# Kernel optimization log

Hardware: AMD Instinct MI355X
Metric: run time of the kernel (lower is better)

## Reference

```python
import jax, jax.numpy as jnp
import numpy as np

BLOCK = 32           # sparsity_config.block
STRIDE_BLOCKS = 4    # stride 128 // block 32
B, H, L, HD = 2, 16, 4096, 64


def _make_fixed_layout(nb, bs):
    """DeepSpeed 'fixed' unidirectional layout, numverts=vertsize=1 (same for all heads)."""
    lay = np.zeros((nb, nb), dtype=np.int64)
    # local: lower-triangular within each stride window
    for i in range(0, nb, bs):
        for j in range(i, i + bs):
            lay[j, i:j + 1] = 1
    # global: vertical stripe at column offset bs-1 of every window, causal (col < row)
    start = bs - 1
    for i in range(nb):
        for j in range(start, i, bs):
            lay[i, j] = 1
    rows, cols = np.nonzero(lay)  # sorted by row
    return jnp.asarray(rows, jnp.int32), jnp.asarray(cols, jnp.int32)


def setup_inputs() -> dict:
    key = jax.random.key(0)
    kq, kk, kv = jax.random.split(key, 3)
    query = jax.random.normal(kq, (B, H, L, HD), jnp.float32)
    key_t = jax.random.normal(kk, (B, H, L, HD), jnp.float32)
    value = jax.random.normal(kv, (B, H, L, HD), jnp.float32)
    rows, cols = _make_fixed_layout(L // BLOCK, STRIDE_BLOCKS)
    return {"query": query, "key": key_t, "value": value,
            "rows": rows, "cols": cols, "block": BLOCK}


def reference(query, key, value, rows, cols, block):
    b, h, l, hd = query.shape
    nb = l // block
    scale = float(hd) ** (-0.5)
    # [nb, B, H, block, hd] with block-row axis leading for gather/scatter
    qb = jnp.moveaxis(query.reshape(b, h, nb, block, hd), 2, 0)
    kb = jnp.moveaxis(key.reshape(b, h, nb, block, hd), 2, 0)
    vb = jnp.moveaxis(value.reshape(b, h, nb, block, hd), 2, 0)
    # sdd: scores only on active blocks -> [nnz, B, H, block, block]
    s = jnp.einsum('nbhqd,nbhkd->nbhqk', qb[rows], kb[cols]) * scale
    # block-sparse softmax over each query row (segment reduce over blocks sharing a row)
    m_blk = s.max(-1)  # [nnz, B, H, block]
    row_max = jnp.full((nb, b, h, block), -jnp.inf, s.dtype).at[rows].max(m_blk)
    e = jnp.exp(s - row_max[rows][..., None])
    denom = jnp.zeros((nb, b, h, block), s.dtype).at[rows].add(e.sum(-1))
    p = e / denom[rows][..., None]
    # dsd: probs @ value, scatter-add into block rows
    ob = jnp.zeros((nb, b, h, block, hd), s.dtype).at[rows].add(
        jnp.einsum('nbhqk,nbhkd->nbhqd', p, vb[cols]))
    return jnp.moveaxis(ob, 0, 2).reshape(b, h, l, hd)
```

## Files before the change

### kernel.cpp

```cpp
#include <hip/hip_runtime.h>
#include <math.h>

#define BH    32
#define LSEQ  4096
#define HD    64
#define BLK   32
#define NB    128
#define NWIN  32
#define QSCALE 0.18033688011112042f

#define KSTR 34
#define VSTR 17

#define RAW_BARRIER() asm volatile("s_waitcnt lgkmcnt(0)\n\ts_barrier" ::: "memory")

typedef _Float16 h2  __attribute__((ext_vector_type(2)));
typedef _Float16 h8  __attribute__((ext_vector_type(8)));
typedef float    f16v __attribute__((ext_vector_type(16)));

static __device__ __forceinline__ h2 pk(float a, float b) {
    return __builtin_bit_cast(h2, __builtin_amdgcn_cvt_pkrtz(a, b));
}
static __device__ __forceinline__ unsigned pku(float a, float b) {
    return __builtin_bit_cast(unsigned, __builtin_amdgcn_cvt_pkrtz(a, b));
}
static __device__ __forceinline__ short h16(float x) {
    return __builtin_bit_cast(short, (_Float16)x);
}
static __device__ __forceinline__ h8 mk8(h2 a, h2 b, h2 c, h2 d) {
    h8 r;
    r[0] = a[0]; r[1] = a[1]; r[2] = b[0]; r[3] = b[1];
    r[4] = c[0]; r[5] = c[1]; r[6] = d[0]; r[7] = d[1];
    return r;
}

__global__ __launch_bounds__(128)
void sparse_attn_r2f(const float* __restrict__ Q, const float* __restrict__ K,
                     const float* __restrict__ V, float* __restrict__ out)
{
    const int id = (int)blockIdx.x;
    const int cc = id & 255;
    const int kk = id >> 8;
    const int v  = cc & 31;
    const int u  = cc >> 5;
    const int bh = u + 8 * kk;
    int w;
    switch (kk) {
        case 0:  w = v;              break;
        case 1:  w = (47 - v) & 31;  break;
        case 2:  w = (v + 16) & 31;  break;
        default: w = (63 - v) & 31;  break;
    }

    const int t    = (int)threadIdx.x;
    const int wid  = t >> 6;
    const int lane = t & 63;
    const int l31  = lane & 31;
    const int h    = lane >> 5;
    const int d0   = 2 * wid, d1 = 2 * wid + 1;
    const int r0   = 4 * w + d0, r1 = r0 + 1;

    __shared__ __align__(16) unsigned kbuf[2][BLK * KSTR];
    __shared__ __align__(16) unsigned vbuf[2][HD * VSTR];

    const size_t base = (size_t)bh * (LSEQ * HD);

    h8 qf0[4], qf1[4];
    {
        const float* qp0 = Q + base + (size_t)(r0 * BLK + l31) * HD + 8 * h;
        const float* qp1 = Q + base + (size_t)(r1 * BLK + l31) * HD + 8 * h;
#pragma unroll
        for (int tt = 0; tt < 4; ++tt) {
            float4 a = *(const float4*)(qp0 + 16 * tt);
            float4 b = *(const float4*)(qp0 + 16 * tt + 4);
            qf0[tt] = mk8(pk(a.x * QSCALE, a.y * QSCALE), pk(a.z * QSCALE, a.w * QSCALE),
                          pk(b.x * QSCALE, b.y * QSCALE), pk(b.z * QSCALE, b.w * QSCALE));
            float4 c = *(const float4*)(qp1 + 16 * tt);
            float4 e = *(const float4*)(qp1 + 16 * tt + 4);
            qf1[tt] = mk8(pk(c.x * QSCALE, c.y * QSCALE), pk(c.z * QSCALE, c.w * QSCALE),
                          pk(e.x * QSCALE, e.y * QSCALE), pk(e.z * QSCALE, e.w * QSCALE));
        }
    }

    f16v o00 = {}, o01 = {}, o10 = {}, o11 = {};
    float2 ls0 = make_float2(0.0f, 0.0f);
    float2 ls1 = make_float2(0.0f, 0.0f);

    const int n    = w + 4;
    const int srow = t >> 2;
    const int sdg  = t & 3;

    const float* kgb = K + base + (size_t)srow * HD + sdg * 16;
    const float* vgb = V + base + (size_t)srow * HD + sdg * 16;

    float4 kq0, kq1, kq2, kq3, vq0, vq1, vq2, vq3;

    auto loadR = [&](int j) {
        const int col = (j < w) ? (4 * j + 3) : (4 * w + (j - w));
        const size_t off = (size_t)col * (BLK * HD);
        kq0 = *(const float4*)(kgb + off);
        kq1 = *(const float4*)(kgb + off + 4);
        kq2 = *(const float4*)(kgb + off + 8);
        kq3 = *(const float4*)(kgb + off + 12);
        vq0 = *(const float4*)(vgb + off);
        vq1 = *(const float4*)(vgb + off + 4);
        vq2 = *(const float4*)(vgb + off + 8);
        vq3 = *(const float4*)(vgb + off + 12);
    };
    auto writeL = [&](int b) {
        unsigned* kb = &kbuf[b][srow * KSTR + sdg * 8];
        uint2 w0, w1, w2, w3;
        w0.x = pku(kq0.x, kq0.y); w0.y = pku(kq0.z, kq0.w);
        w1.x = pku(kq1.x, kq1.y); w1.y = pku(kq1.z, kq1.w);
        w2.x = pku(kq2.x, kq2.y); w2.y = pku(kq2.z, kq2.w);
        w3.x = pku(kq3.x, kq3.y); w3.y = pku(kq3.z, kq3.w);
        *(uint2*)&kb[0] = w0;
        *(uint2*)&kb[2] = w1;
        *(uint2*)&kb[4] = w2;
        *(uint2*)&kb[6] = w3;
        short* vs = (short*)&vbuf[b][0];
        const int vd0 = sdg * 16;
        vs[(vd0 +  0) * (2 * VSTR) + srow] = h16(vq0.x);
        vs[(vd0 +  1) * (2 * VSTR) + srow] = h16(vq0.y);
        vs[(vd0 +  2) * (2 * VSTR) + srow] = h16(vq0.z);
        vs[(vd0 +  3) * (2 * VSTR) + srow] = h16(vq0.w);
        vs[(vd0 +  4) * (2 * VSTR) + srow] = h16(vq1.x);
        vs[(vd0 +  5) * (2 * VSTR) + srow] = h16(vq1.y);
        vs[(vd0 +  6) * (2 * VSTR) + srow] = h16(vq1.z);
        vs[(vd0 +  7) * (2 * VSTR) + srow] = h16(vq1.w);
        vs[(vd0 +  8) * (2 * VSTR) + srow] = h16(vq2.x);
        vs[(vd0 +  9) * (2 * VSTR) + srow] = h16(vq2.y);
        vs[(vd0 + 10) * (2 * VSTR) + srow] = h16(vq2.z);
        vs[(vd0 + 11) * (2 * VSTR) + srow] = h16(vq2.w);
        vs[(vd0 + 12) * (2 * VSTR) + srow] = h16(vq3.x);
        vs[(vd0 + 13) * (2 * VSTR) + srow] = h16(vq3.y);
        vs[(vd0 + 14) * (2 * VSTR) + srow] = h16(vq3.z);
        vs[(vd0 + 15) * (2 * VSTR) + srow] = h16(vq3.w);
    };

    auto smpv = [&](const f16v& st, float2& ls, f16v& oa, f16v& ob,
                    const h8& vf00, const h8& vf01,
                    const h8& vf10, const h8& vf11) {
        float ps[16];
#pragma unroll
        for (int g = 0; g < 16; ++g) ps[g] = __builtin_exp2f(st[g]);
#pragma unroll
        for (int g = 0; g < 8; ++g) {
            ls.x += ps[2 * g];
            ls.y += ps[2 * g + 1];
        }
        h2 ph2[8];
#pragma unroll
        for (int jj = 0; jj < 8; ++jj) ph2[jj] = pk(ps[2 * jj], ps[2 * jj + 1]);
#pragma unroll
        for (int t2 = 0; t2 < 2; ++t2) {
            h2 s0 = h ? ph2[4 * t2]     : ph2[4 * t2 + 2];
            h2 s1 = h ? ph2[4 * t2 + 1] : ph2[4 * t2 + 3];
            int i0 = __shfl_xor(__builtin_bit_cast(int, s0), 32);
            int i1 = __shfl_xor(__builtin_bit_cast(int, s1), 32);
            h2 g0 = __builtin_bit_cast(h2, i0), g1 = __builtin_bit_cast(h2, i1);
            h2 c0 = h ? g0 : ph2[4 * t2];
            h2 c1 = h ? g1 : ph2[4 * t2 + 1];
            h2 c2 = h ? ph2[4 * t2 + 2] : g0;
            h2 c3 = h ? ph2[4 * t2 + 3] : g1;
            h8 pa = mk8(c0, c1, c2, c3);
            oa = __builtin_amdgcn_mfma_f32_32x32x16_f16(pa, t2 ? vf10 : vf00, oa, 0, 0, 0);
            ob = __builtin_amdgcn_mfma_f32_32x32x16_f16(pa, t2 ? vf11 : vf01, ob, 0, 0, 0);
        }
    };

    loadR(0);
    int pb = 0;

    for (int j = 0; j < n; ++j, pb ^= 1) {
        writeL(pb);
        if (j + 1 < n) loadR(j + 1);
        RAW_BARRIER();

        const int jj = j - w;
        const bool act1 = (jj < 0) || (jj <= d1);
        const bool act0 = (jj < 0) || (jj <= d0);
        if (act1) {
            const unsigned* kb = kbuf[pb];
            const unsigned* vb = vbuf[pb];

            f16v st0 = {}, st1 = {};
#pragma unroll
            for (int tt = 0; tt < 4; ++tt) {
                const int kw = l31 * KSTR + 8 * tt + 4 * h;
                uint2 u0 = *(const uint2*)&kb[kw];
                uint2 u1 = *(const uint2*)&kb[kw + 2];
                uint4 uu; uu.x = u0.x; uu.y = u0.y; uu.z = u1.x; uu.w = u1.y;
                h8 kf = __builtin_bit_cast(h8, uu);
                st1 = __builtin_amdgcn_mfma_f32_32x32x16_f16(kf, qf1[tt], st1, 0, 0, 0);
                st0 = __builtin_amdgcn_mfma_f32_32x32x16_f16(kf, qf0[tt], st0, 0, 0, 0);
            }

            const int va = l31 * VSTR + 4 * h;
            const int vc = (32 + l31) * VSTR + 4 * h;
            uint4 x00, x01, x10, x11;
            x00.x = vb[va];     x00.y = vb[va + 1];  x00.z = vb[va + 2];  x00.w = vb[va + 3];
            x01.x = vb[vc];     x01.y = vb[vc + 1];  x01.z = vb[vc + 2];  x01.w = vb[vc + 3];
            x10.x = vb[va + 8]; x10.y = vb[va + 9];  x10.z = vb[va + 10]; x10.w = vb[va + 11];
            x11.x = vb[vc + 8]; x11.y = vb[vc + 9];  x11.z = vb[vc + 10]; x11.w = vb[vc + 11];
            h8 vf00 = __builtin_bit_cast(h8, x00);
            h8 vf01 = __builtin_bit_cast(h8, x01);
            h8 vf10 = __builtin_bit_cast(h8, x10);
            h8 vf11 = __builtin_bit_cast(h8, x11);

            smpv(st1, ls1, o10, o11, vf00, vf01, vf10, vf11);
            if (act0) smpv(st0, ls0, o00, o01, vf00, vf01, vf10, vf11);
        }
    }

    auto finish = [&](float2 ls, const f16v& oa, const f16v& ob, int r) {
        float lsum = ls.x + ls.y;
        lsum += __shfl_xor(lsum, 32);
        const float inv = 1.0f / lsum;
        float* op = out + base + (size_t)(r * BLK) * HD;
#pragma unroll
        for (int g = 0; g < 16; ++g) {
            const int qrow = (g & 3) + 8 * (g >> 2) + 4 * h;
            int iv = __builtin_amdgcn_ds_bpermute(qrow << 2, __float_as_int(inv));
            const float invq = __int_as_float(iv);
            op[(size_t)qrow * HD + l31]      = oa[g] * invq;
            op[(size_t)qrow * HD + 32 + l31] = ob[g] * invq;
        }
    };
    finish(ls0, o00, o01, r0);
    finish(ls1, o10, o11, r1);
}

extern "C" void kernel_launch(void* const* d_in, const int* in_sizes, int n_in,
                              void* d_out, int out_size, void* d_ws, size_t ws_size,
                              hipStream_t stream) {
    const float* Q = (const float*)d_in[0];
    const float* K = (const float*)d_in[1];
    const float* V = (const float*)d_in[2];

    dim3 grid(NWIN * BH);
    dim3 block(128);
    sparse_attn_r2f<<<grid, block, 0, stream>>>(Q, K, V, (float*)d_out);
}
```

Before: 173.7 us.

## Split window work into single-wave blocks with barrier-free LDS double buffering

Each 128-thread block handling four block-rows of a window is replaced by two 64-thread single-wave blocks, each handling two block-rows and iterating only over the column blocks it needs. With one wave per block, the LDS barrier is removed. Global loads are prefetched two steps ahead and LDS writes one step ahead. The V tile row order is permuted so the P-matrix fragment can feed the PV MFMA directly without the cross-lane shuffle. This trades duplicated K/V loading across the two halves for more blocks, less wasted work on the diagonal, and no block-level synchronisation.

After: 172.4 us. Within noise of the previous version (-0.8%).

```diff
diff --git a/kernel.cpp b/kernel.cpp
--- a/kernel.cpp
+++ b/kernel.cpp
@@ -12,8 +12,6 @@
 #define KSTR 34
 #define VSTR 17
 
-#define RAW_BARRIER() asm volatile("s_waitcnt lgkmcnt(0)\n\ts_barrier" ::: "memory")
-
 typedef _Float16 h2  __attribute__((ext_vector_type(2)));
 typedef _Float16 h8  __attribute__((ext_vector_type(8)));
 typedef float    f16v __attribute__((ext_vector_type(16)));
@@ -34,31 +32,35 @@
     return r;
 }
 
-__global__ __launch_bounds__(128)
-void sparse_attn_r2f(const float* __restrict__ Q, const float* __restrict__ K,
-                     const float* __restrict__ V, float* __restrict__ out)
+__global__ __launch_bounds__(64, 2)
+void sparse_attn_pw(const float* __restrict__ Q, const float* __restrict__ K,
+                    const float* __restrict__ V, float* __restrict__ out)
 {
     const int id = (int)blockIdx.x;
     const int cc = id & 255;
-    const int kk = id >> 8;
+    const int s  = id >> 8;
     const int v  = cc & 31;
     const int u  = cc >> 5;
-    const int bh = u + 8 * kk;
+    const int q  = s >> 1;
+    const int half = s & 1;
     int w;
-    switch (kk) {
+    switch (q) {
         case 0:  w = v;              break;
         case 1:  w = (47 - v) & 31;  break;
         case 2:  w = (v + 16) & 31;  break;
         default: w = (63 - v) & 31;  break;
     }
-
-    const int t    = (int)threadIdx.x;
-    const int wid  = t >> 6;
-    const int lane = t & 63;
-    const int l31  = lane & 31;
-    const int h    = lane >> 5;
-    const int d0   = 2 * wid, d1 = 2 * wid + 1;
-    const int r0   = 4 * w + d0, r1 = r0 + 1;
+    const int bh = u + 8 * q;
+
+    const int t   = (int)threadIdx.x;
+    const int l31 = t & 31;
+    const int h   = t >> 5;
+    const int t15 = t & 15;
+    const int tr4 = t >> 4;
+
+    const int d0 = 2 * half, d1 = d0 + 1;
+    const int r0 = 4 * w + d0, r1 = r0 + 1;
+    const int n  = w + 2 + 2 * half;
 
     __shared__ __align__(16) unsigned kbuf[2][BLK * KSTR];
     __shared__ __align__(16) unsigned vbuf[2][HD * VSTR];
@@ -86,61 +88,44 @@
     float2 ls0 = make_float2(0.0f, 0.0f);
     float2 ls1 = make_float2(0.0f, 0.0f);
 
-    const int n    = w + 4;
-    const int srow = t >> 2;
-    const int sdg  = t & 3;
-
-    const float* kgb = K + base + (size_t)srow * HD + sdg * 16;
-    const float* vgb = V + base + (size_t)srow * HD + sdg * 16;
-
-    float4 kq0, kq1, kq2, kq3, vq0, vq1, vq2, vq3;
-
-    auto loadR = [&](int j) {
-        const int col = (j < w) ? (4 * j + 3) : (4 * w + (j - w));
-        const size_t off = (size_t)col * (BLK * HD);
-        kq0 = *(const float4*)(kgb + off);
-        kq1 = *(const float4*)(kgb + off + 4);
-        kq2 = *(const float4*)(kgb + off + 8);
-        kq3 = *(const float4*)(kgb + off + 12);
-        vq0 = *(const float4*)(vgb + off);
-        vq1 = *(const float4*)(vgb + off + 4);
-        vq2 = *(const float4*)(vgb + off + 8);
-        vq3 = *(const float4*)(vgb + off + 12);
+    float4 kst[8], vst[8];
+    const float* kg = K + base + (size_t)(tr4 * HD) + 4 * t15;
+    const float* vg = V + base + (size_t)(tr4 * HD) + 4 * t15;
+
+    auto colOf = [&](int j) { return (j < w) ? (4 * j + 3) : (4 * w + (j - w)); };
+    auto loadG = [&](int j) {
+        const size_t off = (size_t)colOf(j) * (BLK * HD);
+#pragma unroll
+        for (int i = 0; i < 8; ++i) {
+            kst[i] = *(const float4*)(kg + off + i * 4 * HD);
+            vst[i] = *(const float4*)(vg + off + i * 4 * HD);
+        }
     };
     auto writeL = [&](int b) {
-        unsigned* kb = &kbuf[b][srow * KSTR + sdg * 8];
-        uint2 w0, w1, w2, w3;
-        w0.x = pku(kq0.x, kq0.y); w0.y = pku(kq0.z, kq0.w);
-        w1.x = pku(kq1.x, kq1.y); w1.y = pku(kq1.z, kq1.w);
-        w2.x = pku(kq2.x, kq2.y); w2.y = pku(kq2.z, kq2.w);
-        w3.x = pku(kq3.x, kq3.y); w3.y = pku(kq3.z, kq3.w);
-        *(uint2*)&kb[0] = w0;
-        *(uint2*)&kb[2] = w1;
-        *(uint2*)&kb[4] = w2;
-        *(uint2*)&kb[6] = w3;
         short* vs = (short*)&vbuf[b][0];
-        const int vd0 = sdg * 16;
-        vs[(vd0 +  0) * (2 * VSTR) + srow] = h16(vq0.x);
-        vs[(vd0 +  1) * (2 * VSTR) + srow] = h16(vq0.y);
-        vs[(vd0 +  2) * (2 * VSTR) + srow] = h16(vq0.z);
-        vs[(vd0 +  3) * (2 * VSTR) + srow] = h16(vq0.w);
-        vs[(vd0 +  4) * (2 * VSTR) + srow] = h16(vq1.x);
-        vs[(vd0 +  5) * (2 * VSTR) + srow] = h16(vq1.y);
-        vs[(vd0 +  6) * (2 * VSTR) + srow] = h16(vq1.z);
-        vs[(vd0 +  7) * (2 * VSTR) + srow] = h16(vq1.w);
-        vs[(vd0 +  8) * (2 * VSTR) + srow] = h16(vq2.x);
-        vs[(vd0 +  9) * (2 * VSTR) + srow] = h16(vq2.y);
-        vs[(vd0 + 10) * (2 * VSTR) + srow] = h16(vq2.z);
-        vs[(vd0 + 11) * (2 * VSTR) + srow] = h16(vq2.w);
-        vs[(vd0 + 12) * (2 * VSTR) + srow] = h16(vq3.x);
-        vs[(vd0 + 13) * (2 * VSTR) + srow] = h16(vq3.y);
-        vs[(vd0 + 14) * (2 * VSTR) + srow] = h16(vq3.z);
-        vs[(vd0 + 15) * (2 * VSTR) + srow] = h16(vq3.w);
-    };
-
-    auto smpv = [&](const f16v& st, float2& ls, f16v& oa, f16v& ob,
-                    const h8& vf00, const h8& vf01,
-                    const h8& vf10, const h8& vf11) {
+#pragma unroll
+        for (int i = 0; i < 8; ++i) {
+            const int row = tr4 + 4 * i;
+            uint2 kw2;
+            kw2.x = pku(kst[i].x, kst[i].y);
+            kw2.y = pku(kst[i].z, kst[i].w);
+            *(uint2*)&kbuf[b][row * KSTR + 2 * t15] = kw2;
+            const int slot = (row & 19) | ((row & 4) << 1) | ((row & 8) >> 1);
+            vs[(4 * t15 + 0) * (2 * VSTR) + slot] = h16(vst[i].x);
+            vs[(4 * t15 + 1) * (2 * VSTR) + slot] = h16(vst[i].y);
+            vs[(4 * t15 + 2) * (2 * VSTR) + slot] = h16(vst[i].z);
+            vs[(4 * t15 + 3) * (2 * VSTR) + slot] = h16(vst[i].w);
+        }
+    };
+
+    uint4 kr0, kr1, kr2, kr3, vr00, vr01, vr10, vr11;
+    auto tile = [&](const h8 (&qf)[4], f16v& oa, f16v& ob, float2& ls) {
+        f16v st = {};
+        st = __builtin_amdgcn_mfma_f32_32x32x16_f16(__builtin_bit_cast(h8, kr0), qf[0], st, 0, 0, 0);
+        st = __builtin_amdgcn_mfma_f32_32x32x16_f16(__builtin_bit_cast(h8, kr1), qf[1], st, 0, 0, 0);
+        st = __builtin_amdgcn_mfma_f32_32x32x16_f16(__builtin_bit_cast(h8, kr2), qf[2], st, 0, 0, 0);
+        st = __builtin_amdgcn_mfma_f32_32x32x16_f16(__builtin_bit_cast(h8, kr3), qf[3], st, 0, 0, 0);
+
         float ps[16];
 #pragma unroll
         for (int g = 0; g < 16; ++g) ps[g] = __builtin_exp2f(st[g]);
@@ -151,66 +136,52 @@
         }
         h2 ph2[8];
 #pragma unroll
-        for (int jj = 0; jj < 8; ++jj) ph2[jj] = pk(ps[2 * jj], ps[2 * jj + 1]);
-#pragma unroll
-        for (int t2 = 0; t2 < 2; ++t2) {
-            h2 s0 = h ? ph2[4 * t2]     : ph2[4 * t2 + 2];
-            h2 s1 = h ? ph2[4 * t2 + 1] : ph2[4 * t2 + 3];
-            int i0 = __shfl_xor(__builtin_bit_cast(int, s0), 32);
-            int i1 = __shfl_xor(__builtin_bit_cast(int, s1), 32);
-            h2 g0 = __builtin_bit_cast(h2, i0), g1 = __builtin_bit_cast(h2, i1);
-            h2 c0 = h ? g0 : ph2[4 * t2];
-            h2 c1 = h ? g1 : ph2[4 * t2 + 1];
-            h2 c2 = h ? ph2[4 * t2 + 2] : g0;
-            h2 c3 = h ? ph2[4 * t2 + 3] : g1;
-            h8 pa = mk8(c0, c1, c2, c3);
-            oa = __builtin_amdgcn_mfma_f32_32x32x16_f16(pa, t2 ? vf10 : vf00, oa, 0, 0, 0);
-            ob = __builtin_amdgcn_mfma_f32_32x32x16_f16(pa, t2 ? vf11 : vf01, ob, 0, 0, 0);
-        }
-    };
-
-    loadR(0);
+        for (int m = 0; m < 8; ++m) ph2[m] = pk(ps[2 * m], ps[2 * m + 1]);
+
+        h8 pa0 = mk8(ph2[0], ph2[1], ph2[2], ph2[3]);
+        h8 pa1 = mk8(ph2[4], ph2[5], ph2[6], ph2[7]);
+        oa = __builtin_amdgcn_mfma_f32_32x32x16_f16(pa0, __builtin_bit_cast(h8, vr00), oa, 0, 0, 0);
+        ob = __builtin_amdgcn_mfma_f32_32x32x16_f16(pa0, __builtin_bit_cast(h8, vr01), ob, 0, 0, 0);
+        oa = __builtin_amdgcn_mfma_f32_32x32x16_f16(pa1, __builtin_bit_cast(h8, vr10), oa, 0, 0, 0);
+        ob = __builtin_amdgcn_mfma_f32_32x32x16_f16(pa1, __builtin_bit_cast(h8, vr11), ob, 0, 0, 0);
+    };
+
+    loadG(0);
+    writeL(0);
+    loadG(1);
+
     int pb = 0;
-
-    for (int j = 0; j < n; ++j, pb ^= 1) {
-        writeL(pb);
-        if (j + 1 < n) loadR(j + 1);
-        RAW_BARRIER();
-
-        const int jj = j - w;
-        const bool act1 = (jj < 0) || (jj <= d1);
+    for (int bb = 0; bb < n; ++bb, pb ^= 1) {
+        const unsigned* kb = kbuf[pb];
+        const unsigned* vb = vbuf[pb];
+
+        {
+            const int kw = l31 * KSTR + 4 * h;
+            uint2 a, b2;
+            a = *(const uint2*)&kb[kw +  0]; b2 = *(const uint2*)&kb[kw +  2];
+            kr0.x = a.x; kr0.y = a.y; kr0.z = b2.x; kr0.w = b2.y;
+            a = *(const uint2*)&kb[kw +  8]; b2 = *(const uint2*)&kb[kw + 10];
+            kr1.x = a.x; kr1.y = a.y; kr1.z = b2.x; kr1.w = b2.y;
+            a = *(const uint2*)&kb[kw + 16]; b2 = *(const uint2*)&kb[kw + 18];
+            kr2.x = a.x; kr2.y = a.y; kr2.z = b2.x; kr2.w = b2.y;
+            a = *(const uint2*)&kb[kw + 24]; b2 = *(const uint2*)&kb[kw + 26];
+            kr3.x = a.x; kr3.y = a.y; kr3.z = b2.x; kr3.w = b2.y;
+
+            const int va0 = l31 * VSTR + 4 * h;
+            const int va1 = (32 + l31) * VSTR + 4 * h;
+            vr00.x = vb[va0];      vr00.y = vb[va0 + 1];  vr00.z = vb[va0 + 2];  vr00.w = vb[va0 + 3];
+            vr10.x = vb[va0 + 8];  vr10.y = vb[va0 + 9];  vr10.z = vb[va0 + 10]; vr10.w = vb[va0 + 11];
+            vr01.x = vb[va1];      vr01.y = vb[va1 + 1];  vr01.z = vb[va1 + 2];  vr01.w = vb[va1 + 3];
+            vr11.x = vb[va1 + 8];  vr11.y = vb[va1 + 9];  vr11.z = vb[va1 + 10]; vr11.w = vb[va1 + 11];
+        }
+
+        const int jj = bb - w;
         const bool act0 = (jj < 0) || (jj <= d0);
-        if (act1) {
-            const unsigned* kb = kbuf[pb];
-            const unsigned* vb = vbuf[pb];
-
-            f16v st0 = {}, st1 = {};
-#pragma unroll
-            for (int tt = 0; tt < 4; ++tt) {
-                const int kw = l31 * KSTR + 8 * tt + 4 * h;
-                uint2 u0 = *(const uint2*)&kb[kw];
-                uint2 u1 = *(const uint2*)&kb[kw + 2];
-                uint4 uu; uu.x = u0.x; uu.y = u0.y; uu.z = u1.x; uu.w = u1.y;
-                h8 kf = __builtin_bit_cast(h8, uu);
-                st1 = __builtin_amdgcn_mfma_f32_32x32x16_f16(kf, qf1[tt], st1, 0, 0, 0);
-                st0 = __builtin_amdgcn_mfma_f32_32x32x16_f16(kf, qf0[tt], st0, 0, 0, 0);
-            }
-
-            const int va = l31 * VSTR + 4 * h;
-            const int vc = (32 + l31) * VSTR + 4 * h;
-            uint4 x00, x01, x10, x11;
-            x00.x = vb[va];     x00.y = vb[va + 1];  x00.z = vb[va + 2];  x00.w = vb[va + 3];
-            x01.x = vb[vc];     x01.y = vb[vc + 1];  x01.z = vb[vc + 2];  x01.w = vb[vc + 3];
-            x10.x = vb[va + 8]; x10.y = vb[va + 9];  x10.z = vb[va + 10]; x10.w = vb[va + 11];
-            x11.x = vb[vc + 8]; x11.y = vb[vc + 9];  x11.z = vb[vc + 10]; x11.w = vb[vc + 11];
-            h8 vf00 = __builtin_bit_cast(h8, x00);
-            h8 vf01 = __builtin_bit_cast(h8, x01);
-            h8 vf10 = __builtin_bit_cast(h8, x10);
-            h8 vf11 = __builtin_bit_cast(h8, x11);
-
-            smpv(st1, ls1, o10, o11, vf00, vf01, vf10, vf11);
-            if (act0) smpv(st0, ls0, o00, o01, vf00, vf01, vf10, vf11);
-        }
+        tile(qf1, o10, o11, ls1);
+        if (act0) tile(qf0, o00, o01, ls0);
+
+        if (bb + 1 < n) writeL(pb ^ 1);
+        if (bb + 2 < n) loadG(bb + 2);
     }
 
     auto finish = [&](float2 ls, const f16v& oa, const f16v& ob, int r) {
@@ -238,7 +209,7 @@
     const float* K = (const float*)d_in[1];
     const float* V = (const float*)d_in[2];
 
-    dim3 grid(NWIN * BH);
-    dim3 block(128);
-    sparse_attn_r2f<<<grid, block, 0, stream>>>(Q, K, V, (float*)d_out);
-}
+    dim3 grid(NWIN * BH * 2);
+    dim3 block(64);
+    sparse_attn_pw<<<grid, block, 0, stream>>>(Q, K, V, (float*)d_out);
+}
```
